# Optimization experiments

Hardware: AMD Instinct MI355X
Metric: run time of the kernel (lower is better)

The kernel has to match this reference:

```python
import jax, jax.numpy as jnp
import numpy as np
from jax import lax

B, T, IN_DIM, HIDDEN = 8, 4096, 1024, 1024


def setup_inputs() -> dict:
    key = jax.random.key(0)
    k_x, k_wd, k_wb = jax.random.split(key, 3)
    x = jax.random.normal(k_x, (B, T, IN_DIM), dtype=jnp.float32)
    h0 = jnp.zeros((B, HIDDEN), dtype=jnp.float32)
    # nn.Linear default init ~ U(-1/sqrt(in), 1/sqrt(in)); b_proj.weight ~ N(0, 0.02)
    lim = 1.0 / np.sqrt(IN_DIM)
    Wd = jax.random.uniform(k_wd, (HIDDEN, IN_DIM), jnp.float32, -lim, lim)
    bd = jnp.zeros((HIDDEN,), dtype=jnp.float32)
    Wb = 0.02 * jax.random.normal(k_wb, (HIDDEN, IN_DIM), dtype=jnp.float32)
    bb = jnp.zeros((HIDDEN,), dtype=jnp.float32)
    # 'hasani' init: A_log = log(linspace(0.5, 2.0, hidden))
    A_log = jnp.log(jnp.linspace(0.5, 2.0, HIDDEN, dtype=jnp.float32))
    return {"x": x, "h0": h0, "Wd": Wd, "bd": bd, "Wb": Wb, "bb": bb, "A_log": A_log}


def _combine(c1, c2):
    # composition of affine maps h -> a*h + b
    a1, b1 = c1
    a2, b2 = c2
    return a1 * a2, a2 * b1 + b2


def reference(x, h0, Wd, bd, Wb, bb, A_log):
    # projections: (B,T,in) @ (in,hidden)
    delta = jax.nn.softplus(jnp.einsum('bti,hi->bth', x, Wd) + bd)
    b_t = delta * (jnp.einsum('bti,hi->bth', x, Wb) + bb)
    A = jnp.exp(A_log)                      # (H,) decay rate
    A_t = jnp.exp(-delta * A)               # (B,T,H)
    # parallel (Blelloch/Heinsen-style) associative scan over T:
    # cumulative affine maps give h_t = A_cum_t * h0 + B_cum_t
    A_cum, B_cum = lax.associative_scan(_combine, (A_t, b_t), axis=1)
    h_full = A_cum * h0[:, None, :] + B_cum  # (B,T,H)
    return jnp.tanh(h_full)                  # bound=True
```

## Files before the change

kernel.cpp:

```cpp
#include <hip/hip_runtime.h>
#include <math.h>

#define B_DIM 8
#define T_DIM 4096
#define K_DIM 1024
#define H_DIM 1024
#define M_DIM (B_DIM * T_DIM)

#define CH 64
#define NC (T_DIM / CH)
#define BK 64

typedef short bf16x8 __attribute__((ext_vector_type(8)));
typedef float f32x4  __attribute__((ext_vector_type(4)));

__device__ __forceinline__ unsigned short f2bf(float f) {
  unsigned int u = __builtin_bit_cast(unsigned int, f);
  u += 0x7FFFu + ((u >> 16) & 1u);
  return (unsigned short)(u >> 16);
}

__device__ __forceinline__ void gload_lds16(const void* g, void* l) {
  __builtin_amdgcn_global_load_lds(
      (const __attribute__((address_space(1))) unsigned int*)g,
      (__attribute__((address_space(3))) unsigned int*)l,
      16 , 0 , 0 );
}

__device__ __forceinline__ float softplus_fast(float x) {
  float e = __expf(-fabsf(x));
  return fmaxf(x, 0.f) + __logf(1.f + e);
}

__device__ __forceinline__ float tanh_fast(float x) {
  float e = __expf(2.f * x);
  return 1.f - 2.f * __builtin_amdgcn_rcpf(e + 1.f);
}

__global__ __launch_bounds__(256) void k_cvt(const float* __restrict__ in,
                                             unsigned short* __restrict__ out,
                                             int n8) {
  int i = blockIdx.x * 256 + threadIdx.x;
  if (i >= n8) return;
  float4 v0 = ((const float4*)in)[i * 2 + 0];
  float4 v1 = ((const float4*)in)[i * 2 + 1];
  bf16x8 r;
  r[0] = (short)f2bf(v0.x); r[1] = (short)f2bf(v0.y);
  r[2] = (short)f2bf(v0.z); r[3] = (short)f2bf(v0.w);
  r[4] = (short)f2bf(v1.x); r[5] = (short)f2bf(v1.y);
  r[6] = (short)f2bf(v1.z); r[7] = (short)f2bf(v1.w);
  ((bf16x8*)out)[i] = r;
}

__global__ __launch_bounds__(512, 4) void k_gemm_dual(
    const unsigned short* __restrict__ Xb,
    const unsigned short* __restrict__ Wdb,
    const unsigned short* __restrict__ Wbb,
    const float* __restrict__ bd,
    const float* __restrict__ bb,
    const float* __restrict__ A_log,
    float* __restrict__ a_out,
    float* __restrict__ b_out,
    float* __restrict__ aggA,
    float* __restrict__ aggB)
{
  __shared__ unsigned short As [128 * BK];
  __shared__ unsigned short Bs0[128 * BK];
  __shared__ unsigned short Bs1[128 * BK];

  const int tid  = threadIdx.x;
  const int bm   = blockIdx.x * 128;
  const int bn   = blockIdx.y * 128;
  const int w    = tid >> 6;
  const int lane = tid & 63;
  const int wm   = (w >> 2) * 64;
  const int wn   = (w & 3) * 32;

  f32x4 accd[4][2], accb[4][2];
  const f32x4 z4 = {0.f, 0.f, 0.f, 0.f};
  for (int m = 0; m < 4; m++)
    for (int n = 0; n < 2; n++) { accd[m][n] = z4; accb[m][n] = z4; }

  const int fr = lane & 15;
  const int hi = lane >> 4;

  for (int k0 = 0; k0 < K_DIM; k0 += BK) {
#pragma unroll
    for (int i = 0; i < 2; i++) {
      int idx = i * 512 + tid;
      int row = idx >> 3;
      int cg  = (idx & 7) ^ (row & 7);
      size_t goffA = (size_t)(bm + row) * K_DIM + (size_t)(k0 + cg * 8);
      size_t goffB = (size_t)(bn + row) * K_DIM + (size_t)(k0 + cg * 8);
      gload_lds16(Xb  + goffA, (char*)As  + idx * 16);
      gload_lds16(Wdb + goffB, (char*)Bs0 + idx * 16);
      gload_lds16(Wbb + goffB, (char*)Bs1 + idx * 16);
    }
    __syncthreads();

#pragma unroll
    for (int ks = 0; ks < 2; ks++) {
      bf16x8 af[4], b0[2], b1[2];
#pragma unroll
      for (int m = 0; m < 4; m++) {
        int row = wm + m * 16 + fr;
        int ch  = (ks * 4 + hi) ^ (row & 7);
        af[m] = *(const bf16x8*)&As[row * BK + ch * 8];
      }
#pragma unroll
      for (int n = 0; n < 2; n++) {
        int row = wn + n * 16 + fr;
        int ch  = (ks * 4 + hi) ^ (row & 7);
        b0[n] = *(const bf16x8*)&Bs0[row * BK + ch * 8];
        b1[n] = *(const bf16x8*)&Bs1[row * BK + ch * 8];
      }
#pragma unroll
      for (int m = 0; m < 4; m++)
#pragma unroll
        for (int n = 0; n < 2; n++) {
          accd[m][n] = __builtin_amdgcn_mfma_f32_16x16x32_bf16(af[m], b0[n], accd[m][n], 0, 0, 0);
          accb[m][n] = __builtin_amdgcn_mfma_f32_16x16x32_bf16(af[m], b1[n], accb[m][n], 0, 0, 0);
        }
    }
    __syncthreads();
  }

  const int col    = lane & 15;
  const int rbase  = hi * 4;
  const int bidx   = bm >> 12;
  const int cchunk = ((bm & (T_DIM - 1)) + wm) >> 6;

#pragma unroll
  for (int n = 0; n < 2; n++) {
    int gn = bn + wn + n * 16 + col;
    float bdv = bd[gn];
    float bbv = bb[gn];
    float Ah  = __expf(A_log[gn]);
    float segA[4], segB[4];
#pragma unroll
    for (int m = 0; m < 4; m++) {
      float sA = 1.f, sB = 0.f;
#pragma unroll
      for (int r = 0; r < 4; r++) {
        int gm = bm + wm + m * 16 + rbase + r;
        float z1  = accd[m][n][r] + bdv;
        float z2  = accb[m][n][r] + bbv;
        float dlt = softplus_fast(z1);
        float av  = __expf(-dlt * Ah);
        float bv  = dlt * z2;
        size_t off = (size_t)gm * H_DIM + (size_t)gn;
        a_out[off] = av;
        b_out[off] = bv;
        sB = fmaf(av, sB, bv);
        sA *= av;
      }
      segA[m] = sA; segB[m] = sB;
    }
    float chA = 1.f, chB = 0.f;
#pragma unroll
    for (int m = 0; m < 4; m++) {
#pragma unroll
      for (int h2 = 0; h2 < 4; h2++) {
        float sa = __shfl(segA[m], col + h2 * 16, 64);
        float sb = __shfl(segB[m], col + h2 * 16, 64);
        chB = fmaf(sa, chB, sb);
        chA *= sa;
      }
    }
    if (lane < 16) {
      size_t o = ((size_t)(bidx * NC + cchunk) << 10) + (size_t)gn;
      aggA[o] = chA;
      aggB[o] = chB;
    }
  }
}

__global__ __launch_bounds__(256) void k_scan_chunks(
    const float* __restrict__ aggA, const float* __restrict__ aggB,
    const float* __restrict__ h0, float* __restrict__ hstart)
{
  int idx = blockIdx.x * 256 + threadIdx.x;
  int h   = idx & (H_DIM - 1);
  int b   = idx >> 10;
  float hc = h0[idx];
  for (int c = 0; c < NC; c++) {
    size_t o = ((size_t)(b * NC + c) << 10) + (size_t)h;
    hstart[o] = hc;
    hc = fmaf(aggA[o], hc, aggB[o]);
  }
}

__global__ __launch_bounds__(256) void k_scan_apply(
    const float* __restrict__ a_arr, const float* b_arr,
    const float* __restrict__ hstart, float* out)
{
  int idx = blockIdx.x * 256 + threadIdx.x;
  int h   = idx & (H_DIM - 1);
  int bc  = idx >> 10;
  int c   = bc & (NC - 1);
  int b   = bc >> 6;
  size_t base = ((size_t)b * T_DIM + (size_t)c * CH) * H_DIM + (size_t)h;
  float hc = hstart[idx];
#pragma unroll 4
  for (int i = 0; i < CH; i++) {
    size_t o = base + (size_t)i * H_DIM;
    float at = a_arr[o];
    float bt = b_arr[o];
    hc = fmaf(at, hc, bt);
    out[o] = tanh_fast(hc);
  }
}

extern "C" void kernel_launch(void* const* d_in, const int* in_sizes, int n_in,
                              void* d_out, int out_size, void* d_ws, size_t ws_size,
                              hipStream_t stream) {
  const float* x     = (const float*)d_in[0];
  const float* h0    = (const float*)d_in[1];
  const float* Wd    = (const float*)d_in[2];
  const float* bd    = (const float*)d_in[3];
  const float* Wb    = (const float*)d_in[4];
  const float* bb    = (const float*)d_in[5];
  const float* A_log = (const float*)d_in[6];
  float* out = (float*)d_out;

  char* ws = (char*)d_ws;
  unsigned short* xb   = (unsigned short*)(ws + 0);
  unsigned short* wdb  = (unsigned short*)(ws + 67108864);
  unsigned short* wbb  = (unsigned short*)(ws + 69206016);
  float*          aarr = (float*)(ws + 71303168);
  float*          aggA = (float*)(ws + 205520896);
  float*          aggB = (float*)(ws + 207618048);
  float*          hst  = (float*)(ws + 209715200);
  float*          barr = out;

  k_cvt<<<(M_DIM * K_DIM / 8) / 256, 256, 0, stream>>>(x, xb, M_DIM * K_DIM / 8);
  k_cvt<<<(H_DIM * K_DIM / 8) / 256, 256, 0, stream>>>(Wd, wdb, H_DIM * K_DIM / 8);
  k_cvt<<<(H_DIM * K_DIM / 8) / 256, 256, 0, stream>>>(Wb, wbb, H_DIM * K_DIM / 8);

  dim3 gg(M_DIM / 128, H_DIM / 128);
  k_gemm_dual<<<gg, 512, 0, stream>>>(xb, wdb, wbb, bd, bb, A_log,
                                      aarr, barr, aggA, aggB);

  k_scan_chunks<<<(B_DIM * H_DIM) / 256,      256, 0, stream>>>(aggA, aggB, h0, hst);
  k_scan_apply <<<(B_DIM * NC * H_DIM) / 256, 256, 0, stream>>>(aarr, barr, hst, out);
}
```

Measured before the change: 337.0 us.

## Double-buffer GEMM LDS tiles and remap workgroups for XCD locality

Switches the dual GEMM to double-buffered LDS, so the global-to-LDS loads for the next K step are issued before computing the current one, and drops one barrier per iteration. Also flattens the grid and remaps block IDs so each XCD handles a contiguous range of M rows across all 8 N tiles, aiming for better L2 reuse of X tiles. LDS use doubles to 96KB per block, and launch bounds drop to 2 blocks per SM, which lowers occupancy.

```diff
diff --git a/kernel.cpp b/kernel.cpp
--- a/kernel.cpp
+++ b/kernel.cpp
@@ -10,6 +10,7 @@
 #define CH 64
 #define NC (T_DIM / CH)
 #define BK 64
+#define NKS (K_DIM / BK)
 
 typedef short bf16x8 __attribute__((ext_vector_type(8)));
 typedef float f32x4  __attribute__((ext_vector_type(4)));
@@ -52,7 +53,7 @@
   ((bf16x8*)out)[i] = r;
 }
 
-__global__ __launch_bounds__(512, 4) void k_gemm_dual(
+__global__ __launch_bounds__(512, 2) void k_gemm_dual(
     const unsigned short* __restrict__ Xb,
     const unsigned short* __restrict__ Wdb,
     const unsigned short* __restrict__ Wbb,
@@ -64,13 +65,17 @@
     float* __restrict__ aggA,
     float* __restrict__ aggB)
 {
-  __shared__ unsigned short As [128 * BK];
-  __shared__ unsigned short Bs0[128 * BK];
-  __shared__ unsigned short Bs1[128 * BK];
+  __shared__ unsigned short As [2][128 * BK];
+  __shared__ unsigned short Bs0[2][128 * BK];
+  __shared__ unsigned short Bs1[2][128 * BK];
 
   const int tid  = threadIdx.x;
-  const int bm   = blockIdx.x * 128;
-  const int bn   = blockIdx.y * 128;
+  const int wgid = blockIdx.x;
+  const int xcd  = wgid & 7;
+  const int j    = wgid >> 3;
+  const int bm   = (xcd * 32 + (j >> 3)) * 128;
+  const int bn   = (j & 7) * 128;
+
   const int w    = tid >> 6;
   const int lane = tid & 63;
   const int wm   = (w >> 2) * 64;
@@ -84,7 +89,7 @@
   const int fr = lane & 15;
   const int hi = lane >> 4;
 
-  for (int k0 = 0; k0 < K_DIM; k0 += BK) {
+  auto stage = [&](int buf, int k0) {
 #pragma unroll
     for (int i = 0; i < 2; i++) {
       int idx = i * 512 + tid;
@@ -92,12 +97,13 @@
       int cg  = (idx & 7) ^ (row & 7);
       size_t goffA = (size_t)(bm + row) * K_DIM + (size_t)(k0 + cg * 8);
       size_t goffB = (size_t)(bn + row) * K_DIM + (size_t)(k0 + cg * 8);
-      gload_lds16(Xb  + goffA, (char*)As  + idx * 16);
-      gload_lds16(Wdb + goffB, (char*)Bs0 + idx * 16);
-      gload_lds16(Wbb + goffB, (char*)Bs1 + idx * 16);
-    }
-    __syncthreads();
-
+      gload_lds16(Xb  + goffA, (char*)As [buf] + idx * 16);
+      gload_lds16(Wdb + goffB, (char*)Bs0[buf] + idx * 16);
+      gload_lds16(Wbb + goffB, (char*)Bs1[buf] + idx * 16);
+    }
+  };
+
+  auto compute = [&](int buf) {
 #pragma unroll
     for (int ks = 0; ks < 2; ks++) {
       bf16x8 af[4], b0[2], b1[2];
@@ -105,14 +111,14 @@
       for (int m = 0; m < 4; m++) {
         int row = wm + m * 16 + fr;
         int ch  = (ks * 4 + hi) ^ (row & 7);
-        af[m] = *(const bf16x8*)&As[row * BK + ch * 8];
+        af[m] = *(const bf16x8*)&As[buf][row * BK + ch * 8];
       }
 #pragma unroll
       for (int n = 0; n < 2; n++) {
         int row = wn + n * 16 + fr;
         int ch  = (ks * 4 + hi) ^ (row & 7);
-        b0[n] = *(const bf16x8*)&Bs0[row * BK + ch * 8];
-        b1[n] = *(const bf16x8*)&Bs1[row * BK + ch * 8];
+        b0[n] = *(const bf16x8*)&Bs0[buf][row * BK + ch * 8];
+        b1[n] = *(const bf16x8*)&Bs1[buf][row * BK + ch * 8];
       }
 #pragma unroll
       for (int m = 0; m < 4; m++)
@@ -122,7 +128,18 @@
           accb[m][n] = __builtin_amdgcn_mfma_f32_16x16x32_bf16(af[m], b1[n], accb[m][n], 0, 0, 0);
         }
     }
+  };
+
+  stage(0, 0);
+  __syncthreads();
+
+  int cur = 0;
+#pragma unroll 1
+  for (int t = 0; t < NKS; ++t) {
+    if (t + 1 < NKS) stage(cur ^ 1, (t + 1) * BK);
+    compute(cur);
     __syncthreads();
+    cur ^= 1;
   }
 
   const int col    = lane & 15;
@@ -237,9 +254,8 @@
   k_cvt<<<(H_DIM * K_DIM / 8) / 256, 256, 0, stream>>>(Wd, wdb, H_DIM * K_DIM / 8);
   k_cvt<<<(H_DIM * K_DIM / 8) / 256, 256, 0, stream>>>(Wb, wbb, H_DIM * K_DIM / 8);
 
-  dim3 gg(M_DIM / 128, H_DIM / 128);
-  k_gemm_dual<<<gg, 512, 0, stream>>>(xb, wdb, wbb, bd, bb, A_log,
-                                      aarr, barr, aggA, aggB);
+  k_gemm_dual<<<(M_DIM / 128) * (H_DIM / 128), 512, 0, stream>>>(
+      xb, wdb, wbb, bd, bb, A_log, aarr, barr, aggA, aggB);
 
   k_scan_chunks<<<(B_DIM * H_DIM) / 256,      256, 0, stream>>>(aggA, aggB, h0, hst);
   k_scan_apply <<<(B_DIM * NC * H_DIM) / 256, 256, 0, stream>>>(aarr, barr, hst, out);
```

Result: slower. 411.7 us (+22.2%).
